# Kernel tuning notes

Measured on AMD Instinct MI355X. Metric: run time of the kernel, lower is better.

The kernel has to match this reference:

```python
import jax, jax.numpy as jnp
import numpy as np

N_QUAT = 4
VERONESE_DIM = 10
OUT_FEATURES = 132

# static index sets matching torch.triu_indices(4, 4)
_rows, _cols = np.triu_indices(N_QUAT)          # 10 upper-tri entries
_mask = _rows != _cols
TRIU_ROWS = jnp.asarray(_rows)
TRIU_COLS = jnp.asarray(_cols)
SYM_ROWS = jnp.asarray(_cols[_mask])            # mirrored lower-tri
SYM_COLS = jnp.asarray(_rows[_mask])
SYM_Z_IDX = jnp.asarray(np.nonzero(_mask)[0])


def setup_inputs() -> dict:
    key = jax.random.key(0)
    k_z, k_w1, k_w2 = jax.random.split(key, 3)
    B, D_IN, D_HID, D_OUT_NN = 65536, 256, 1024, 128
    z = jax.random.normal(k_z, (B, D_IN), dtype=jnp.float32)
    W1 = jax.random.normal(k_w1, (D_IN, D_HID), dtype=jnp.float32) * 0.02
    b1 = jnp.zeros((D_HID,), dtype=jnp.float32)
    W2 = jax.random.normal(k_w2, (D_HID, D_OUT_NN), dtype=jnp.float32) * 0.02
    b2 = jnp.zeros((D_OUT_NN,), dtype=jnp.float32)
    return {"z": z, "W1": W1, "b1": b1, "W2": W2, "b2": b2}


def _recover_quat(z_v):
    # z_v: (B, 10) -> symmetric (B, 4, 4) -> top eigenvector -> (B, 4)
    B = z_v.shape[0]
    M = jnp.zeros((B, N_QUAT, N_QUAT), dtype=z_v.dtype)
    M = M.at[:, TRIU_ROWS, TRIU_COLS].set(z_v)
    M = M.at[:, SYM_ROWS, SYM_COLS].set(z_v[:, SYM_Z_IDX])
    _, vecs = jnp.linalg.eigh(M)          # eigenvalues ascending
    q = vecs[:, :, -1]                    # eigenvector of largest eigenvalue
    sign = jnp.sign(q[:, 0:1] + 1e-9)
    return q * sign


def reference(z, W1, b1, W2, b2):
    orig_shape = z.shape
    zf = z.reshape(-1, orig_shape[-1])           # (B, in_features)
    q_pred = _recover_quat(zf[:, :VERONESE_DIM])  # (B, 4)
    h = jax.nn.relu(zf @ W1 + b1)
    others = h @ W2 + b2                          # (B, 128)
    B = zf.shape[0]
    out = jnp.zeros((B, OUT_FEATURES), dtype=zf.dtype)
    out = out.at[:, :N_QUAT].set(q_pred)          # quat_indices = [0,1,2,3]
    out = out.at[:, N_QUAT:].set(others)          # non_quat = [4..131]
    return out.reshape(*orig_shape[:-1], OUT_FEATURES)
```

## Files before the change

kernel.cpp:

```cpp
#include <hip/hip_runtime.h>


typedef short s16x8 __attribute__((ext_vector_type(8)));
typedef float f32x4 __attribute__((ext_vector_type(4)));
typedef unsigned char u8;

__device__ __forceinline__ f32x4 mfma16(s16x8 a, s16x8 b, f32x4 c) {
    return __builtin_amdgcn_mfma_f32_16x16x32_bf16(a, b, c, 0, 0, 0);
}

__device__ __forceinline__ short f2bf(float f) {
    unsigned int u = __float_as_uint(f);
    u = (u + 0x7fffu + ((u >> 16) & 1u)) >> 16;
    return (short)u;
}

__device__ __forceinline__ unsigned cvt_pk(float lo, float hi) {
    unsigned r;
    asm("v_cvt_pk_bf16_f32 %0, %1, %2" : "=v"(r) : "v"(lo), "v"(hi));
    return r;
}

__device__ __forceinline__ void gload_lds16(const void* g, void* l) {
    __builtin_amdgcn_global_load_lds(
        (const __attribute__((address_space(1))) unsigned int*)g,
        (__attribute__((address_space(3))) unsigned int*)l, 16, 0, 0);
}

__global__ __launch_bounds__(256) void prep_weights(
    const float* __restrict__ W1, const float* __restrict__ W2,
    uint4* __restrict__ w1t, uint4* __restrict__ w2t)
{
    int tid = blockIdx.x * 256 + threadIdx.x;
    int q = (tid >> 4) & 3, r16 = tid & 15;
    union { short b[8]; uint4 v; } pk;
    if (tid < 32768) {
        int s  = (tid >> 6) & 7;
        int ct = (tid >> 9) & 3;
        int c  = tid >> 11;
        int k0 = s * 32 + q * 8;
        int n1 = c * 64 + ct * 16 + r16;
        #pragma unroll
        for (int j = 0; j < 8; ++j)
            pk.b[j] = f2bf(W1[(k0 + j) * 1024 + n1]);
        w1t[tid] = pk.v;
    } else {
        int f   = tid - 32768;
        int ct2 = (f >> 6) & 7;
        int s2  = (f >> 9) & 1;
        int c   = f >> 10;
        int k0  = c * 64 + s2 * 32 + q * 8;
        int n2  = ct2 * 16 + r16;
        #pragma unroll
        for (int j = 0; j < 8; ++j)
            pk.b[j] = f2bf(W2[(k0 + j) * 128 + n2]);
        w2t[f] = pk.v;
    }
}

__global__ __launch_bounds__(256, 1) void fused_all(
    const float* __restrict__ z, const float* __restrict__ b1,
    const float* __restrict__ b2, const uint4* __restrict__ w1t,
    const uint4* __restrict__ w2t, float* __restrict__ out)
{
    __shared__ __align__(16) u8 lds[135168];

    const int t    = threadIdx.x;
    const int lane = t & 63;
    const int w    = t >> 6;
    const int q    = lane >> 4;
    const int r16  = lane & 15;
    const int bm0  = blockIdx.x * 256;
    const int rowbase = bm0 + w * 64;

    #pragma unroll
    for (int i = 0; i < 8; ++i) {
        int f = i * 256 + t;
        gload_lds16(w1t + f, lds + f * 16);
    }
    #pragma unroll
    for (int i = 0; i < 4; ++i) {
        int f = i * 256 + t;
        gload_lds16(w2t + f, lds + 65536 + f * 16);
    }
    gload_lds16(b1 + t * 4, lds + 131072 + t * 16);

    {
        int row = rowbase + lane;
        const float* zr = z + (size_t)row * 256;
        float4 v0 = *(const float4*)(zr);
        float4 v1 = *(const float4*)(zr + 4);
        float2 v2 = *(const float2*)(zr + 8);

        float A[4][4] = {{v0.x, v0.y, v0.z, v0.w},
                         {v0.y, v1.x, v1.y, v1.z},
                         {v0.z, v1.y, v1.w, v2.x},
                         {v0.w, v1.z, v2.x, v2.y}};
        float V[4][4] = {{1.f, 0.f, 0.f, 0.f},
                         {0.f, 1.f, 0.f, 0.f},
                         {0.f, 0.f, 1.f, 0.f},
                         {0.f, 0.f, 0.f, 1.f}};

#define ROT(p, qq) do {                                                   \
        float apq  = A[p][qq];                                            \
        float tau  = (A[qq][qq] - A[p][p]) *                              \
                     __builtin_amdgcn_rcpf(2.0f * apq);                   \
        float tt   = __builtin_amdgcn_rcpf(                               \
                        fabsf(tau) +                                      \
                        __builtin_amdgcn_sqrtf(fmaf(tau, tau, 1.0f)));    \
        tt = copysignf(tt, tau);                                          \
        tt = (fabsf(apq) > 1e-20f) ? tt : 0.0f;                           \
        float cth = __builtin_amdgcn_rsqf(fmaf(tt, tt, 1.0f));            \
        float sth = tt * cth;                                             \
        _Pragma("unroll")                                                 \
        for (int k = 0; k < 4; ++k) {                                     \
            float akp = A[k][p], akq = A[k][qq];                          \
            A[k][p]  = cth * akp - sth * akq;                             \
            A[k][qq] = sth * akp + cth * akq;                             \
        }                                                                 \
        _Pragma("unroll")                                                 \
        for (int k = 0; k < 4; ++k) {                                     \
            float apk = A[p][k], aqk = A[qq][k];                          \
            A[p][k]  = cth * apk - sth * aqk;                             \
            A[qq][k] = sth * apk + cth * aqk;                             \
        }                                                                 \
        _Pragma("unroll")                                                 \
        for (int k = 0; k < 4; ++k) {                                     \
            float vkp = V[k][p], vkq = V[k][qq];                          \
            V[k][p]  = cth * vkp - sth * vkq;                             \
            V[k][qq] = sth * vkp + cth * vkq;                             \
        }                                                                 \
    } while (0)

        #pragma unroll 1
        for (int sweep = 0; sweep < 6; ++sweep) {
            ROT(0, 1); ROT(0, 2); ROT(0, 3); ROT(1, 2); ROT(1, 3); ROT(2, 3);
        }
#undef ROT

        float bv = A[0][0];
        float q0 = V[0][0], q1 = V[1][0], q2 = V[2][0], q3 = V[3][0];
        #pragma unroll
        for (int k = 1; k < 4; ++k) {
            bool better = A[k][k] > bv;
            bv = better ? A[k][k] : bv;
            q0 = better ? V[0][k] : q0;
            q1 = better ? V[1][k] : q1;
            q2 = better ? V[2][k] : q2;
            q3 = better ? V[3][k] : q3;
        }
        float sgn = (q0 + 1e-9f) >= 0.0f ? 1.0f : -1.0f;
        *(float4*)(out + (size_t)row * 132) =
            make_float4(sgn * q0, sgn * q1, sgn * q2, sgn * q3);
    }

    const f32x4 zero4 = {0.f, 0.f, 0.f, 0.f};
    s16x8 zf[4][8];
    #pragma unroll
    for (int mr = 0; mr < 4; ++mr) {
        const float* zp = z + (size_t)(rowbase + mr * 16 + r16) * 256 + q * 8;
        #pragma unroll
        for (int s = 0; s < 8; ++s) {
            const float4* p = (const float4*)(zp + s * 32);
            float4 a0 = p[0], a1 = p[1];
            union { unsigned u[4]; s16x8 v; } pk;
            pk.u[0] = cvt_pk(a0.x, a0.y);
            pk.u[1] = cvt_pk(a0.z, a0.w);
            pk.u[2] = cvt_pk(a1.x, a1.y);
            pk.u[3] = cvt_pk(a1.z, a1.w);
            zf[mr][s] = pk.v;
        }
    }

    f32x4 acc2[4][8];
    #pragma unroll
    for (int mr = 0; mr < 4; ++mr)
        #pragma unroll
        for (int n = 0; n < 8; ++n) acc2[mr][n] = zero4;

    __syncthreads();

    const u8* const aW0 = lds + lane * 16;
    const u8* const aW1 = lds + 32768 + lane * 16;
    const u8* const bW0 = lds + 65536 + lane * 16;
    const u8* const bW1 = lds + 81920 + lane * 16;
    u8* const hwv = lds + 98304 + w * 8192;
    u8* const hwr = hwv + r16 * 16 + ((q >> 1) << 8) + ((q & 1) << 3);
    const u8* const hrd = hwv + lane * 16;
    const u8* const blsp = lds + 131072 + q * 16;

    auto chunk = [&](int c, const u8* a, const u8* bW,
                     u8* s1dst, u8* s2dst) {
        if (c < 15) {
            const uint4* s1 = w1t + (c + 1) * 2048;
            const uint4* s2 = w2t + (c + 1) * 1024;
            #pragma unroll
            for (int i = 0; i < 8; ++i) {
                int f = i * 256 + t;
                gload_lds16(s1 + f, s1dst + f * 16);
            }
            #pragma unroll
            for (int i = 0; i < 4; ++i) {
                int f = i * 256 + t;
                gload_lds16(s2 + f, s2dst + f * 16);
            }
        }

        __builtin_amdgcn_s_setprio(1);

        #pragma unroll
        for (int ct = 0; ct < 4; ++ct) {
            f32x4 ac0 = zero4, ac1 = zero4, ac2 = zero4, ac3 = zero4;
            #pragma unroll
            for (int s = 0; s < 8; ++s) {
                s16x8 afr = *(const s16x8*)(a + (ct * 8 + s) * 1024);
                ac0 = mfma16(afr, zf[0][s], ac0);
                ac1 = mfma16(afr, zf[1][s], ac1);
                ac2 = mfma16(afr, zf[2][s], ac2);
                ac3 = mfma16(afr, zf[3][s], ac3);
            }
            f32x4 bv = *(const f32x4*)(blsp + c * 256 + ct * 64);
            #pragma unroll
            for (int mr = 0; mr < 4; ++mr) {
                f32x4 av = (mr == 0) ? ac0 : (mr == 1) ? ac1
                         : (mr == 2) ? ac2 : ac3;
                uint2 hp;
                hp.x = cvt_pk(fmaxf(av[0] + bv[0], 0.f),
                              fmaxf(av[1] + bv[1], 0.f));
                hp.y = cvt_pk(fmaxf(av[2] + bv[2], 0.f),
                              fmaxf(av[3] + bv[3], 0.f));
                *(uint2*)(hwr + mr * 2048 + ct * 512) = hp;
            }
        }

        #pragma unroll
        for (int s2 = 0; s2 < 2; ++s2) {
            s16x8 af0 = *(const s16x8*)(hrd + s2 * 1024);
            s16x8 af1 = *(const s16x8*)(hrd + 2048 + s2 * 1024);
            s16x8 af2 = *(const s16x8*)(hrd + 4096 + s2 * 1024);
            s16x8 af3 = *(const s16x8*)(hrd + 6144 + s2 * 1024);
            #pragma unroll
            for (int ct2 = 0; ct2 < 8; ++ct2) {
                s16x8 bfr = *(const s16x8*)(bW + (s2 * 8 + ct2) * 1024);
                acc2[0][ct2] = mfma16(af0, bfr, acc2[0][ct2]);
                acc2[1][ct2] = mfma16(af1, bfr, acc2[1][ct2]);
                acc2[2][ct2] = mfma16(af2, bfr, acc2[2][ct2]);
                acc2[3][ct2] = mfma16(af3, bfr, acc2[3][ct2]);
            }
        }

        __builtin_amdgcn_s_setprio(0);

        __syncthreads();
    };

    u8* const s1b0 = lds;
    u8* const s1b1 = lds + 32768;
    u8* const s2b0 = lds + 65536;
    u8* const s2b1 = lds + 81920;

    #pragma unroll 1
    for (int cc = 0; cc < 8; ++cc) {
        chunk(2 * cc,     aW0, bW0, s1b1, s2b1);
        chunk(2 * cc + 1, aW1, bW1, s1b0, s2b0);
    }

    #pragma unroll
    for (int ct2 = 0; ct2 < 8; ++ct2) {
        const float b2v = b2[ct2 * 16 + r16];
        #pragma unroll
        for (int mr = 0; mr < 4; ++mr) {
            #pragma unroll
            for (int r = 0; r < 4; ++r) {
                int m = w * 64 + mr * 16 + q * 4 + r;
                out[(size_t)(bm0 + m) * 132 + 4 + ct2 * 16 + r16] =
                    acc2[mr][ct2][r] + b2v;
            }
        }
    }
}

extern "C" void kernel_launch(void* const* d_in, const int* in_sizes, int n_in,
                              void* d_out, int out_size, void* d_ws, size_t ws_size,
                              hipStream_t stream) {
    const float* z  = (const float*)d_in[0];
    const float* W1 = (const float*)d_in[1];
    const float* b1 = (const float*)d_in[2];
    const float* W2 = (const float*)d_in[3];
    const float* b2 = (const float*)d_in[4];
    float* out = (float*)d_out;

    uint4* w1t = (uint4*)d_ws;
    uint4* w2t = (uint4*)((char*)d_ws + 512 * 1024);

    hipLaunchKernelGGL(prep_weights, dim3(192), dim3(256), 0, stream,
                       W1, W2, w1t, w2t);
    hipLaunchKernelGGL(fused_all, dim3(256), dim3(256), 0, stream,
                       z, b1, b2, (const uint4*)w1t, (const uint4*)w2t, out);
}
```

Measured before the change: 81.90 us.

## Switch to 32x32 MFMA with register-resident hidden tile and two blocks per CU

Replaces the 16x16x32 bf16 MFMA with 32x32x16 tiles and halves rows per block (128) so two blocks fit per CU with a smaller LDS footprint. The hidden activation no longer round-trips through LDS; it is repacked in registers with v_permlane32_swap into the A-operand layout for the second GEMM. W2 fragments are now read directly from global memory (L2) instead of being staged in LDS. The second-GEMM MFMAs are interleaved with the first-GEMM tiles. The aim is higher occupancy and less LDS traffic, at the cost of duplicated W1 streaming per block and global-latency W2 loads.

```diff
diff --git a/kernel.cpp b/kernel.cpp
--- a/kernel.cpp
+++ b/kernel.cpp
@@ -3,10 +3,11 @@
 
 typedef short s16x8 __attribute__((ext_vector_type(8)));
 typedef float f32x4 __attribute__((ext_vector_type(4)));
+typedef float f32x16 __attribute__((ext_vector_type(16)));
 typedef unsigned char u8;
 
-__device__ __forceinline__ f32x4 mfma16(s16x8 a, s16x8 b, f32x4 c) {
-    return __builtin_amdgcn_mfma_f32_16x16x32_bf16(a, b, c, 0, 0, 0);
+__device__ __forceinline__ f32x16 mfma32(s16x8 a, s16x8 b, f32x16 c) {
+    return __builtin_amdgcn_mfma_f32_32x32x16_bf16(a, b, c, 0, 0, 0);
 }
 
 __device__ __forceinline__ short f2bf(float f) {
@@ -19,6 +20,10 @@
     unsigned r;
     asm("v_cvt_pk_bf16_f32 %0, %1, %2" : "=v"(r) : "v"(lo), "v"(hi));
     return r;
+}
+
+__device__ __forceinline__ void pl32swap(unsigned& a, unsigned& b) {
+    asm("v_permlane32_swap_b32 %0, %1" : "+v"(a), "+v"(b));
 }
 
 __device__ __forceinline__ void gload_lds16(const void* g, void* l) {
@@ -32,60 +37,54 @@
     uint4* __restrict__ w1t, uint4* __restrict__ w2t)
 {
     int tid = blockIdx.x * 256 + threadIdx.x;
-    int q = (tid >> 4) & 3, r16 = tid & 15;
+    int hl = (tid >> 5) & 1, r32 = tid & 31;
     union { short b[8]; uint4 v; } pk;
     if (tid < 32768) {
-        int s  = (tid >> 6) & 7;
-        int ct = (tid >> 9) & 3;
+        int s  = (tid >> 6) & 15;
+        int ct = (tid >> 10) & 1;
         int c  = tid >> 11;
-        int k0 = s * 32 + q * 8;
-        int n1 = c * 64 + ct * 16 + r16;
+        int k0 = s * 16 + hl * 8;
+        int n1 = c * 64 + ct * 32 + r32;
         #pragma unroll
         for (int j = 0; j < 8; ++j)
             pk.b[j] = f2bf(W1[(k0 + j) * 1024 + n1]);
         w1t[tid] = pk.v;
     } else {
-        int f   = tid - 32768;
-        int ct2 = (f >> 6) & 7;
-        int s2  = (f >> 9) & 1;
-        int c   = f >> 10;
-        int k0  = c * 64 + s2 * 32 + q * 8;
-        int n2  = ct2 * 16 + r16;
+        int g  = tid - 32768;
+        int nt = (g >> 6) & 3;
+        int K  = g >> 8;
+        int k0 = K * 16 + hl * 8;
+        int n2 = nt * 32 + r32;
         #pragma unroll
         for (int j = 0; j < 8; ++j)
             pk.b[j] = f2bf(W2[(k0 + j) * 128 + n2]);
-        w2t[f] = pk.v;
-    }
-}
-
-__global__ __launch_bounds__(256, 1) void fused_all(
+        w2t[g] = pk.v;
+    }
+}
+
+__global__ __launch_bounds__(256, 2) void fused_all(
     const float* __restrict__ z, const float* __restrict__ b1,
     const float* __restrict__ b2, const uint4* __restrict__ w1t,
     const uint4* __restrict__ w2t, float* __restrict__ out)
 {
-    __shared__ __align__(16) u8 lds[135168];
+    __shared__ __align__(16) u8 lds[69632];
 
     const int t    = threadIdx.x;
     const int lane = t & 63;
     const int w    = t >> 6;
-    const int q    = lane >> 4;
-    const int r16  = lane & 15;
-    const int bm0  = blockIdx.x * 256;
-    const int rowbase = bm0 + w * 64;
+    const int hl   = lane >> 5;
+    const int r32  = lane & 31;
+    const int bm0  = blockIdx.x * 128;
+    const int rowbase = bm0 + w * 32;
 
     #pragma unroll
     for (int i = 0; i < 8; ++i) {
         int f = i * 256 + t;
         gload_lds16(w1t + f, lds + f * 16);
     }
-    #pragma unroll
-    for (int i = 0; i < 4; ++i) {
-        int f = i * 256 + t;
-        gload_lds16(w2t + f, lds + 65536 + f * 16);
-    }
-    gload_lds16(b1 + t * 4, lds + 131072 + t * 16);
-
-    {
+    gload_lds16(b1 + t * 4, lds + 65536 + t * 16);
+
+    if (lane < 32) {
         int row = rowbase + lane;
         const float* zr = z + (size_t)row * 256;
         float4 v0 = *(const float4*)(zr);
@@ -154,128 +153,129 @@
             make_float4(sgn * q0, sgn * q1, sgn * q2, sgn * q3);
     }
 
-    const f32x4 zero4 = {0.f, 0.f, 0.f, 0.f};
-    s16x8 zf[4][8];
-    #pragma unroll
-    for (int mr = 0; mr < 4; ++mr) {
-        const float* zp = z + (size_t)(rowbase + mr * 16 + r16) * 256 + q * 8;
-        #pragma unroll
-        for (int s = 0; s < 8; ++s) {
-            const float4* p = (const float4*)(zp + s * 32);
-            float4 a0 = p[0], a1 = p[1];
+    s16x8 zf[16];
+    {
+        const float* zp = z + (size_t)(rowbase + r32) * 256 + hl * 8;
+        #pragma unroll
+        for (int s = 0; s < 16; ++s) {
+            float4 a0 = *(const float4*)(zp + s * 16);
+            float4 a1 = *(const float4*)(zp + s * 16 + 4);
             union { unsigned u[4]; s16x8 v; } pk;
             pk.u[0] = cvt_pk(a0.x, a0.y);
             pk.u[1] = cvt_pk(a0.z, a0.w);
             pk.u[2] = cvt_pk(a1.x, a1.y);
             pk.u[3] = cvt_pk(a1.z, a1.w);
-            zf[mr][s] = pk.v;
-        }
-    }
-
-    f32x4 acc2[4][8];
+            zf[s] = pk.v;
+        }
+    }
+
+    const f32x16 zero16 = {0.f,0.f,0.f,0.f, 0.f,0.f,0.f,0.f,
+                           0.f,0.f,0.f,0.f, 0.f,0.f,0.f,0.f};
+    f32x16 acc2[4];
     #pragma unroll
-    for (int mr = 0; mr < 4; ++mr)
-        #pragma unroll
-        for (int n = 0; n < 8; ++n) acc2[mr][n] = zero4;
+    for (int nt = 0; nt < 4; ++nt) acc2[nt] = zero16;
 
     __syncthreads();
 
-    const u8* const aW0 = lds + lane * 16;
-    const u8* const aW1 = lds + 32768 + lane * 16;
-    const u8* const bW0 = lds + 65536 + lane * 16;
-    const u8* const bW1 = lds + 81920 + lane * 16;
-    u8* const hwv = lds + 98304 + w * 8192;
-    u8* const hwr = hwv + r16 * 16 + ((q >> 1) << 8) + ((q & 1) << 3);
-    const u8* const hrd = hwv + lane * 16;
-    const u8* const blsp = lds + 131072 + q * 16;
-
-    auto chunk = [&](int c, const u8* a, const u8* bW,
-                     u8* s1dst, u8* s2dst) {
+    const u8* const aW0  = lds + lane * 16;
+    const u8* const aW1  = lds + 32768 + lane * 16;
+    const u8* const blsp = lds + 65536 + hl * 16;
+    const s16x8* const w2b = (const s16x8*)w2t + lane;
+
+    u8* const s1b0 = lds;
+    u8* const s1b1 = lds + 32768;
+
+    auto chunk = [&](int c, const u8* a, u8* s1dst) {
+        const s16x8* w2c = w2b + c * 1024;
+        s16x8 w2f[4][4];
+        #pragma unroll
+        for (int ks = 0; ks < 2; ++ks)
+            #pragma unroll
+            for (int nt = 0; nt < 4; ++nt)
+                w2f[ks][nt] = w2c[(ks * 4 + nt) * 64];
+
         if (c < 15) {
             const uint4* s1 = w1t + (c + 1) * 2048;
-            const uint4* s2 = w2t + (c + 1) * 1024;
             #pragma unroll
             for (int i = 0; i < 8; ++i) {
                 int f = i * 256 + t;
                 gload_lds16(s1 + f, s1dst + f * 16);
             }
-            #pragma unroll
-            for (int i = 0; i < 4; ++i) {
-                int f = i * 256 + t;
-                gload_lds16(s2 + f, s2dst + f * 16);
+        }
+
+        const u8* bb = blsp + c * 256;
+        s16x8 hf[4];
+
+        auto tile = [&](int ct) {
+            __builtin_amdgcn_s_setprio(1);
+            f32x16 d = zero16;
+            #pragma unroll
+            for (int s = 0; s < 16; ++s) {
+                s16x8 afr = *(const s16x8*)(a + (ct * 16 + s) * 1024);
+                d = mfma32(afr, zf[s], d);
             }
-        }
-
+            __builtin_amdgcn_s_setprio(0);
+            unsigned Plo[4], Phi[4];
+            #pragma unroll
+            for (int g = 0; g < 4; ++g) {
+                f32x4 bv = *(const f32x4*)(bb + ct * 128 + g * 32);
+                Plo[g] = cvt_pk(fmaxf(d[4*g+0] + bv[0], 0.f),
+                                fmaxf(d[4*g+1] + bv[1], 0.f));
+                Phi[g] = cvt_pk(fmaxf(d[4*g+2] + bv[2], 0.f),
+                                fmaxf(d[4*g+3] + bv[3], 0.f));
+            }
+            #pragma unroll
+            for (int f = 0; f < 2; ++f) {
+                unsigned a0 = Plo[2*f], b0 = Plo[2*f+1];
+                unsigned a1 = Phi[2*f], b1 = Phi[2*f+1];
+                pl32swap(a0, b0);
+                pl32swap(a1, b1);
+                union { unsigned u[4]; s16x8 v; } fr;
+                fr.u[0] = a0; fr.u[1] = a1; fr.u[2] = b0; fr.u[3] = b1;
+                hf[ct * 2 + f] = fr.v;
+            }
+        };
+
+        tile(0);
+        #pragma unroll
+        for (int ks = 2; ks < 4; ++ks)
+            #pragma unroll
+            for (int nt = 0; nt < 4; ++nt)
+                w2f[ks][nt] = w2c[(ks * 4 + nt) * 64];
         __builtin_amdgcn_s_setprio(1);
-
-        #pragma unroll
-        for (int ct = 0; ct < 4; ++ct) {
-            f32x4 ac0 = zero4, ac1 = zero4, ac2 = zero4, ac3 = zero4;
-            #pragma unroll
-            for (int s = 0; s < 8; ++s) {
-                s16x8 afr = *(const s16x8*)(a + (ct * 8 + s) * 1024);
-                ac0 = mfma16(afr, zf[0][s], ac0);
-                ac1 = mfma16(afr, zf[1][s], ac1);
-                ac2 = mfma16(afr, zf[2][s], ac2);
-                ac3 = mfma16(afr, zf[3][s], ac3);
-            }
-            f32x4 bv = *(const f32x4*)(blsp + c * 256 + ct * 64);
-            #pragma unroll
-            for (int mr = 0; mr < 4; ++mr) {
-                f32x4 av = (mr == 0) ? ac0 : (mr == 1) ? ac1
-                         : (mr == 2) ? ac2 : ac3;
-                uint2 hp;
-                hp.x = cvt_pk(fmaxf(av[0] + bv[0], 0.f),
-                              fmaxf(av[1] + bv[1], 0.f));
-                hp.y = cvt_pk(fmaxf(av[2] + bv[2], 0.f),
-                              fmaxf(av[3] + bv[3], 0.f));
-                *(uint2*)(hwr + mr * 2048 + ct * 512) = hp;
-            }
-        }
-
-        #pragma unroll
-        for (int s2 = 0; s2 < 2; ++s2) {
-            s16x8 af0 = *(const s16x8*)(hrd + s2 * 1024);
-            s16x8 af1 = *(const s16x8*)(hrd + 2048 + s2 * 1024);
-            s16x8 af2 = *(const s16x8*)(hrd + 4096 + s2 * 1024);
-            s16x8 af3 = *(const s16x8*)(hrd + 6144 + s2 * 1024);
-            #pragma unroll
-            for (int ct2 = 0; ct2 < 8; ++ct2) {
-                s16x8 bfr = *(const s16x8*)(bW + (s2 * 8 + ct2) * 1024);
-                acc2[0][ct2] = mfma16(af0, bfr, acc2[0][ct2]);
-                acc2[1][ct2] = mfma16(af1, bfr, acc2[1][ct2]);
-                acc2[2][ct2] = mfma16(af2, bfr, acc2[2][ct2]);
-                acc2[3][ct2] = mfma16(af3, bfr, acc2[3][ct2]);
-            }
-        }
-
+        #pragma unroll
+        for (int ks = 0; ks < 2; ++ks)
+            #pragma unroll
+            for (int nt = 0; nt < 4; ++nt)
+                acc2[nt] = mfma32(hf[ks], w2f[ks][nt], acc2[nt]);
+        __builtin_amdgcn_s_setprio(0);
+
+        tile(1);
+        __builtin_amdgcn_s_setprio(1);
+        #pragma unroll
+        for (int ks = 2; ks < 4; ++ks)
+            #pragma unroll
+            for (int nt = 0; nt < 4; ++nt)
+                acc2[nt] = mfma32(hf[ks], w2f[ks][nt], acc2[nt]);
         __builtin_amdgcn_s_setprio(0);
 
         __syncthreads();
     };
 
-    u8* const s1b0 = lds;
-    u8* const s1b1 = lds + 32768;
-    u8* const s2b0 = lds + 65536;
-    u8* const s2b1 = lds + 81920;
-
     #pragma unroll 1
     for (int cc = 0; cc < 8; ++cc) {
-        chunk(2 * cc,     aW0, bW0, s1b1, s2b1);
-        chunk(2 * cc + 1, aW1, bW1, s1b0, s2b0);
+        chunk(2 * cc,     aW0, s1b1);
+        chunk(2 * cc + 1, aW1, s1b0);
     }
 
     #pragma unroll
-    for (int ct2 = 0; ct2 < 8; ++ct2) {
-        const float b2v = b2[ct2 * 16 + r16];
-        #pragma unroll
-        for (int mr = 0; mr < 4; ++mr) {
-            #pragma unroll
-            for (int r = 0; r < 4; ++r) {
-                int m = w * 64 + mr * 16 + q * 4 + r;
-                out[(size_t)(bm0 + m) * 132 + 4 + ct2 * 16 + r16] =
-                    acc2[mr][ct2][r] + b2v;
-            }
+    for (int nt = 0; nt < 4; ++nt) {
+        const float b2v = b2[nt * 32 + r32];
+        #pragma unroll
+        for (int r = 0; r < 16; ++r) {
+            int m = w * 32 + (r & 3) + 8 * (r >> 2) + 4 * hl;
+            out[(size_t)(bm0 + m) * 132 + 4 + nt * 32 + r32] =
+                acc2[nt][r] + b2v;
         }
     }
 }
@@ -295,6 +295,6 @@
 
     hipLaunchKernelGGL(prep_weights, dim3(192), dim3(256), 0, stream,
                        W1, W2, w1t, w2t);
-    hipLaunchKernelGGL(fused_all, dim3(256), dim3(256), 0, stream,
+    hipLaunchKernelGGL(fused_all, dim3(512), dim3(256), 0, stream,
                        z, b1, b2, (const uint4*)w1t, (const uint4*)w2t, out);
 }
```

Result: faster. 73.13 us (-10.7%).
